# Performance work log

Hardware: AMD Instinct MI355X
Metric: run time of the kernel (lower is better)

The kernel has to match this reference:

```python
import jax, jax.numpy as jnp
import numpy as np

B, NV, H, D = 8, 16, 192, 512
NH = 8
HD = D // NH
DFF = 2048
EPS = 1e-5


def _bn(x, g, b):
    # x: (N, T, C); BatchNorm1d over channel C using batch stats (train mode)
    mu = jnp.mean(x, axis=(0, 1))
    var = jnp.var(x, axis=(0, 1))
    return (x - mu) / jnp.sqrt(var + EPS) * g + b


def _ff(x, w1, b1, w2, b2):
    h = jax.nn.gelu(jnp.einsum('bnhd,fd->bnhf', x, w1) + b1, approximate=False)
    return jnp.einsum('bnhf,df->bnhd', h, w2) + b2


def setup_inputs() -> dict:
    key = jax.random.key(0)
    ks = jax.random.split(key, 20)
    s = 0.02
    return {
        'src': jax.random.normal(ks[0], (B, NV, H, D), jnp.float32),
        'qk_w': jax.random.normal(ks[1], (2 * D, D), jnp.float32) * s,
        'qk_b': jnp.zeros((2 * D,), jnp.float32),
        'v_w': jax.random.normal(ks[2], (D, D), jnp.float32) * s,
        'v_b': jnp.zeros((D,), jnp.float32),
        'alpha_p': jax.random.normal(ks[3], (HD, 1), jnp.float32) * 0.1,
        'g_pre1': jnp.ones((D,), jnp.float32),
        'b_pre1': jnp.zeros((D,), jnp.float32),
        'g_pre2': jnp.ones((D,), jnp.float32),
        'b_pre2': jnp.zeros((D,), jnp.float32),
        'ff1_w1': jax.random.normal(ks[4], (DFF, D), jnp.float32) * s,
        'ff1_b1': jnp.zeros((DFF,), jnp.float32),
        'ff1_w2': jax.random.normal(ks[5], (D, DFF), jnp.float32) * s,
        'ff1_b2': jnp.zeros((D,), jnp.float32),
        'ff2_w1': jax.random.normal(ks[6], (DFF, D), jnp.float32) * s,
        'ff2_b1': jnp.zeros((DFF,), jnp.float32),
        'ff2_w2': jax.random.normal(ks[7], (D, DFF), jnp.float32) * s,
        'ff2_b2': jnp.zeros((D,), jnp.float32),
        'g_attn': jnp.ones((D,), jnp.float32),
        'b_attn': jnp.zeros((D,), jnp.float32),
    }


def reference(src, qk_w, qk_b, v_w, v_b, alpha_p,
              g_pre1, b_pre1, g_pre2, b_pre2,
              ff1_w1, ff1_b1, ff1_w2, ff1_b2,
              ff2_w1, ff2_b1, ff2_w2, ff2_b2,
              g_attn, b_attn):
    b, n, h, c = src.shape
    hd = c // NH
    # normalized input for q,k; raw for v
    src1 = src / jnp.linalg.norm(src, axis=-1, keepdims=True)
    qk = (jnp.einsum('bnhc,ec->bnhe', src1, qk_w) + qk_b)
    qk = qk.reshape(b, n, h, 2, NH, hd).transpose(3, 0, 1, 4, 2, 5)  # (2,b,n,NH,h,hd)
    q, k = qk[0], qk[1]
    v = (jnp.einsum('bnhc,ec->bnhe', src, v_w) + v_b)
    v = v.reshape(b, n, h, NH, hd).transpose(0, 1, 3, 2, 4)  # (b,n,NH,h,hd)

    # exponential-decay weights in FFT domain (branch: h != 7)
    a = jax.nn.sigmoid(alpha_p)                  # (hd,1)
    ar = jnp.arange(h - 1, -1, -1, dtype=src.dtype)
    weights = a * (1.0 - a) ** ar                # (hd, h)
    n2 = 2 * h
    w_f = jnp.fft.rfft(weights, n=n2, axis=-1)   # (hd, h+1)
    q_f = jnp.swapaxes(jnp.fft.rfft(q, n=n2, axis=-2), -1, -2) * w_f
    k_f = jnp.swapaxes(jnp.fft.rfft(k, n=n2, axis=-2), -1, -2) * w_f
    q1 = jnp.swapaxes(jnp.fft.irfft(q_f, n=n2, axis=-1)[..., :h], -1, -2)
    k1 = jnp.swapaxes(jnp.fft.irfft(k_f, n=n2, axis=-1)[..., :h], -1, -2)

    # token-axis attention (note: original divides by head_dim**-0.5 == * sqrt(hd))
    score_t = jnp.einsum('bnhed,bnhfd->bnhef', q1, k1) * (hd ** 0.5)
    attn_t = jax.nn.softmax(score_t, axis=-1)
    out_tok = jnp.einsum('bnhef,bnhfd->bnhed', attn_t, v)  # (b,n,NH,h,hd)
    o3 = _bn(out_tok.reshape(b * n, h, NH * hd), g_pre2, b_pre2).reshape(b, n, h, c)

    # hidden-axis attention on un-decayed q,k (scale = sqrt(h))
    score_h = jnp.einsum('bnhae,bnhaf->bnhef', q, k) * (h ** 0.5)
    attn_h = jax.nn.softmax(score_h, axis=-1)
    out_hid = jnp.einsum('bnhef,bnhaf->bnhae', attn_h, v)  # (b,n,NH,h,hd)
    o2 = _bn(out_hid.reshape(b * n, h, NH * hd), g_pre1, b_pre1).reshape(b, n, h, c)

    src2 = _ff(o3, ff1_w1, ff1_b1, ff1_w2, ff1_b2) + _ff(o2, ff2_w1, ff2_b1, ff2_w2, ff2_b2)
    out = src + src2
    out = _bn(out.reshape(b * n, h, c), g_attn, b_attn).reshape(b, n, h, c)
    return out
```

## Files before the change

kernel.cpp:

```cpp
#include <hip/hip_runtime.h>
#include <math.h>

#define SEQ 192
#define NTOK 24576
#define EPS 1e-5f

typedef __bf16 bf16x8 __attribute__((ext_vector_type(8)));
typedef __bf16 bf16x4 __attribute__((ext_vector_type(4)));
typedef float  f32x4  __attribute__((ext_vector_type(4)));

__device__ __forceinline__ void load_lds16(const __bf16* g, __bf16* l) {
    __builtin_amdgcn_global_load_lds(
        (const __attribute__((address_space(1))) uint32_t*)g,
        (__attribute__((address_space(3))) uint32_t*)l, 16, 0, 0);
}

__device__ __forceinline__ float gelu_f(float x) {
    float z = 1.5957691216057308f * x * fmaf(0.044715f, x*x, 1.f);
    float e = __expf(-z);
    return x * __builtin_amdgcn_rcpf(1.f + e);
}

__global__ __launch_bounds__(256) void cvt_k(const float* __restrict__ x, __bf16* __restrict__ y)
{
    int i = blockIdx.x * 256 + threadIdx.x;
    f32x4 v = ((const f32x4*)x)[i];
    bf16x4 o;
    o[0]=(__bf16)v[0]; o[1]=(__bf16)v[1]; o[2]=(__bf16)v[2]; o[3]=(__bf16)v[3];
    ((bf16x4*)y)[i] = o;
}

__global__ __launch_bounds__(256) void prep_k(const float* __restrict__ src,
    __bf16* __restrict__ srcb, __bf16* __restrict__ srcnb)
{
    int w = threadIdx.x >> 6, lane = threadIdx.x & 63;
    size_t token = blockIdx.x * 4 + w;
    const float* p = src + token * 512 + lane * 8;
    f32x4 a0 = *(const f32x4*)p;
    f32x4 a1 = *(const f32x4*)(p + 4);
    float s = a0[0]*a0[0]+a0[1]*a0[1]+a0[2]*a0[2]+a0[3]*a0[3]
            + a1[0]*a1[0]+a1[1]*a1[1]+a1[2]*a1[2]+a1[3]*a1[3];
#pragma unroll
    for (int off = 32; off; off >>= 1) s += __shfl_xor(s, off);
    float rs = rsqrtf(s);
    bf16x8 vb, vn;
#pragma unroll
    for (int q = 0; q < 4; q++) {
        vb[q]   = (__bf16)a0[q];      vn[q]   = (__bf16)(a0[q]*rs);
        vb[q+4] = (__bf16)a1[q];      vn[q+4] = (__bf16)(a1[q]*rs);
    }
    *(bf16x8*)&srcb[token*512 + lane*8]  = vb;
    *(bf16x8*)&srcnb[token*512 + lane*8] = vn;
}

template<bool AFFINE, bool GELU>
__global__ __launch_bounds__(256) void gemm_k(
    const __bf16* __restrict__ A, const __bf16* __restrict__ B, __bf16* __restrict__ C,
    int N, int K, const float* __restrict__ bias, const float* __restrict__ coef)
{
    __shared__ __bf16 As[8192];
    __shared__ __bf16 Bs[8192];
    const int tid = threadIdx.x, lane = tid & 63, w = tid >> 6;
    const int wr = w >> 1, wc = w & 1;
    const int m0 = blockIdx.y * 128, n0 = blockIdx.x * 128;
    const int fr = lane & 15, fq = lane >> 4;
    const int grow = 8*w + (lane >> 3);
    const int gcol = ((lane & 7) ^ (lane >> 3)) * 8;
    const __bf16* gB = B + (size_t)(n0 + grow) * K + gcol;
    const __bf16* gA = A + (size_t)(m0 + grow) * K + gcol;
    __bf16* ldsA = As + 8*w*64 + lane*8;
    __bf16* ldsB = Bs + 8*w*64 + lane*8;

    f32x4 acc[4][4];
#pragma unroll
    for (int i = 0; i < 4; i++)
#pragma unroll
        for (int j = 0; j < 4; j++) acc[i][j] = (f32x4){0.f,0.f,0.f,0.f};

    for (int k0 = 0; k0 < K; k0 += 64) {
        if (!AFFINE) {
#pragma unroll
            for (int i = 0; i < 4; i++)
                load_lds16(gA + k0 + (size_t)(32*i)*K, ldsA + i*2048);
        } else {
            const int r = tid >> 3, cseg = tid & 7;
            const float* scp = coef + k0 + cseg*8;
            const float* shp = coef + 512 + k0 + cseg*8;
            f32x4 sc0 = *(const f32x4*)scp, sc1 = *(const f32x4*)(scp+4);
            f32x4 sh0 = *(const f32x4*)shp, sh1 = *(const f32x4*)(shp+4);
#pragma unroll
            for (int i = 0; i < 4; i++) {
                int row = 32*i + r;
                bf16x8 a = *(const bf16x8*)&A[(size_t)(m0+row)*512 + k0 + cseg*8];
                bf16x8 v;
#pragma unroll
                for (int q = 0; q < 4; q++) {
                    v[q]   = (__bf16)fmaf((float)a[q],   sc0[q], sh0[q]);
                    v[q+4] = (__bf16)fmaf((float)a[q+4], sc1[q], sh1[q]);
                }
                *(bf16x8*)&As[row*64 + ((cseg ^ (r & 7)) * 8)] = v;
            }
        }
#pragma unroll
        for (int i = 0; i < 4; i++)
            load_lds16(gB + k0 + (size_t)(32*i)*K, ldsB + i*2048);
        __syncthreads();
#pragma unroll
        for (int kk = 0; kk < 2; kk++) {
            bf16x8 af[4], bfv[4];
#pragma unroll
            for (int i = 0; i < 4; i++)
                af[i] = *(bf16x8*)&As[(wr*64 + i*16 + fr)*64 + (((kk*4+fq) ^ (fr&7))*8)];
#pragma unroll
            for (int j = 0; j < 4; j++)
                bfv[j] = *(bf16x8*)&Bs[(wc*64 + j*16 + fr)*64 + (((kk*4+fq) ^ (fr&7))*8)];
#pragma unroll
            for (int i = 0; i < 4; i++)
#pragma unroll
                for (int j = 0; j < 4; j++)
                    acc[i][j] = __builtin_amdgcn_mfma_f32_16x16x32_bf16(af[i], bfv[j], acc[i][j], 0, 0, 0);
        }
        __syncthreads();
    }
    const int r4 = lane >> 4, cc = lane & 15;
#pragma unroll
    for (int i = 0; i < 4; i++) {
#pragma unroll
        for (int r = 0; r < 4; r++) {
            int m = m0 + wr*64 + i*16 + r4*4 + r;
#pragma unroll
            for (int j = 0; j < 4; j++) {
                int n = n0 + wc*64 + j*16 + cc;
                float v = acc[i][j][r] + bias[n];
                if (GELU) v = gelu_f(v);
                C[(size_t)m * N + n] = (__bf16)v;
            }
        }
    }
}

__global__ __launch_bounds__(256) void gemm2_k(
    const __bf16* __restrict__ A1, const __bf16* __restrict__ A2,
    const __bf16* __restrict__ B1, const __bf16* __restrict__ B2,
    float* __restrict__ C, const float* __restrict__ b1, const float* __restrict__ b2,
    const float* __restrict__ resid, float* __restrict__ st)
{
    __shared__ __bf16 As[8192];
    __shared__ __bf16 Bs[8192];
    const int tid = threadIdx.x, lane = tid & 63, w = tid >> 6;
    const int wr = w >> 1, wc = w & 1;
    const int m0 = blockIdx.y * 128, n0 = blockIdx.x * 128;
    const int fr = lane & 15, fq = lane >> 4;
    const int grow = 8*w + (lane >> 3);
    const int gcol = ((lane & 7) ^ (lane >> 3)) * 8;
    const int K = 2048;
    __bf16* ldsA = As + 8*w*64 + lane*8;
    __bf16* ldsB = Bs + 8*w*64 + lane*8;

    f32x4 acc[4][4];
#pragma unroll
    for (int i = 0; i < 4; i++)
#pragma unroll
        for (int j = 0; j < 4; j++) acc[i][j] = (f32x4){0.f,0.f,0.f,0.f};

#pragma unroll 1
    for (int half = 0; half < 2; half++) {
        const __bf16* gA = (half ? A2 : A1) + (size_t)(m0 + grow) * K + gcol;
        const __bf16* gB = (half ? B2 : B1) + (size_t)(n0 + grow) * K + gcol;
        for (int k0 = 0; k0 < K; k0 += 64) {
#pragma unroll
            for (int i = 0; i < 4; i++) {
                load_lds16(gA + k0 + (size_t)(32*i)*K, ldsA + i*2048);
                load_lds16(gB + k0 + (size_t)(32*i)*K, ldsB + i*2048);
            }
            __syncthreads();
#pragma unroll
            for (int kk = 0; kk < 2; kk++) {
                bf16x8 af[4], bfv[4];
#pragma unroll
                for (int i = 0; i < 4; i++)
                    af[i] = *(bf16x8*)&As[(wr*64 + i*16 + fr)*64 + (((kk*4+fq) ^ (fr&7))*8)];
#pragma unroll
                for (int j = 0; j < 4; j++)
                    bfv[j] = *(bf16x8*)&Bs[(wc*64 + j*16 + fr)*64 + (((kk*4+fq) ^ (fr&7))*8)];
#pragma unroll
                for (int i = 0; i < 4; i++)
#pragma unroll
                    for (int j = 0; j < 4; j++)
                        acc[i][j] = __builtin_amdgcn_mfma_f32_16x16x32_bf16(af[i], bfv[j], acc[i][j], 0, 0, 0);
            }
            __syncthreads();
        }
    }
    const int r4 = lane >> 4, cc = lane & 15;
    float cs[4] = {0,0,0,0}, cq[4] = {0,0,0,0};
#pragma unroll
    for (int i = 0; i < 4; i++) {
#pragma unroll
        for (int r = 0; r < 4; r++) {
            int m = m0 + wr*64 + i*16 + r4*4 + r;
#pragma unroll
            for (int j = 0; j < 4; j++) {
                int n = n0 + wc*64 + j*16 + cc;
                size_t idx = (size_t)m * 512 + n;
                float v = acc[i][j][r] + b1[n] + b2[n] + resid[idx];
                C[idx] = v;
                cs[j] += v; cq[j] = fmaf(v, v, cq[j]);
            }
        }
    }
#pragma unroll
    for (int j = 0; j < 4; j++) {
        cs[j] += __shfl_xor(cs[j], 16); cs[j] += __shfl_xor(cs[j], 32);
        cq[j] += __shfl_xor(cq[j], 16); cq[j] += __shfl_xor(cq[j], 32);
    }
    if (r4 == 0) {
#pragma unroll
        for (int j = 0; j < 4; j++) {
            int n = n0 + wc*64 + j*16 + cc;
            atomicAdd(&st[n], cs[j]);
            atomicAdd(&st[512 + n], cq[j]);
        }
    }
}

__global__ __launch_bounds__(256) void decay_scan_k(__bf16* __restrict__ QKb, const float* __restrict__ alpha)
{
    int g = blockIdx.x * 256 + threadIdx.x;
    int bn = g >> 10, e = g & 1023;
    float a = 1.f / (1.f + expf(-alpha[e & 63]));
    float rr = 1.f - a;
    __bf16* p = QKb + (size_t)bn * SEQ * 1024 + e;
    float P = 0.f, pw = 1.f;
    for (int t = 0; t < SEQ; t++) {
        P += pw * (float)p[(size_t)t*1024];
        p[(size_t)t*1024] = (__bf16)P;
        pw *= rr;
    }
    float f = a;
    for (int t = SEQ-1; t >= 0; t--) {
        p[(size_t)t*1024] = (__bf16)((float)p[(size_t)t*1024] * f);
        f *= rr;
    }
}

__global__ __launch_bounds__(256) void hidden_attn_mfma_k(
    const __bf16* __restrict__ QKb, const __bf16* __restrict__ Vb, __bf16* __restrict__ OHb)
{
    __shared__ __bf16 smem[25600];
    __bf16* Qt = smem;
    __bf16* Kt = smem + 12800;
    __bf16* Ps = smem;
    __bf16* Vs = smem + 4608;
    const int bn = blockIdx.x >> 3, nh = blockIdx.x & 7;
    const int tid = threadIdx.x, lane = tid & 63, w = tid >> 6;
    const int fr = lane & 15, fq = lane >> 4;
    const size_t rowbase = (size_t)bn * SEQ;

    for (int i = tid; i < 12288; i += 256) {
        int t = i >> 6, j = i & 63;
        const __bf16* g = QKb + (rowbase + t)*1024 + nh*64 + j;
        Qt[j*200 + t] = g[0];
        Kt[j*200 + t] = g[512];
    }
    __syncthreads();

    f32x4 acc[4];
#pragma unroll
    for (int i = 0; i < 4; i++) acc[i] = (f32x4){0.f,0.f,0.f,0.f};
#pragma unroll
    for (int kc = 0; kc < 6; kc++) {
        bf16x8 a = *(bf16x8*)&Qt[(w*16 + fr)*200 + kc*32 + fq*8];
#pragma unroll
        for (int nt = 0; nt < 4; nt++) {
            bf16x8 b = *(bf16x8*)&Kt[(nt*16 + fr)*200 + kc*32 + fq*8];
            acc[nt] = __builtin_amdgcn_mfma_f32_16x16x32_bf16(a, b, acc[nt], 0, 0, 0);
        }
    }
    const float sc = 13.856406460551018f;
    float pn[4][4];
#pragma unroll
    for (int reg = 0; reg < 4; reg++) {
        float m = -1e30f;
#pragma unroll
        for (int nt = 0; nt < 4; nt++) { acc[nt][reg] *= sc; m = fmaxf(m, acc[nt][reg]); }
#pragma unroll
        for (int off = 1; off < 16; off <<= 1) m = fmaxf(m, __shfl_xor(m, off));
        float l = 0.f;
#pragma unroll
        for (int nt = 0; nt < 4; nt++) { pn[nt][reg] = __expf(acc[nt][reg] - m); l += pn[nt][reg]; }
#pragma unroll
        for (int off = 1; off < 16; off <<= 1) l += __shfl_xor(l, off);
        float inv = 1.f / l;
#pragma unroll
        for (int nt = 0; nt < 4; nt++) pn[nt][reg] *= inv;
    }
    __syncthreads();
#pragma unroll
    for (int nt = 0; nt < 4; nt++)
#pragma unroll
        for (int reg = 0; reg < 4; reg++)
            Ps[(w*16 + fq*4 + reg)*72 + nt*16 + fr] = (__bf16)pn[nt][reg];
    for (int i = tid; i < 1536; i += 256) {
        int t = i >> 3, s = i & 7;
        *(bf16x8*)&Vs[t*72 + s*8] = *(const bf16x8*)&Vb[(rowbase+t)*512 + nh*64 + s*8];
    }
    __syncthreads();

    f32x4 o[3][4];
#pragma unroll
    for (int i = 0; i < 3; i++)
#pragma unroll
        for (int j = 0; j < 4; j++) o[i][j] = (f32x4){0.f,0.f,0.f,0.f};
#pragma unroll
    for (int kc = 0; kc < 2; kc++) {
        bf16x8 av[3];
#pragma unroll
        for (int mt = 0; mt < 3; mt++)
            av[mt] = *(bf16x8*)&Vs[(48*w + mt*16 + fr)*72 + kc*32 + fq*8];
#pragma unroll
        for (int nt = 0; nt < 4; nt++) {
            bf16x8 b = *(bf16x8*)&Ps[(nt*16 + fr)*72 + kc*32 + fq*8];
#pragma unroll
            for (int mt = 0; mt < 3; mt++)
                o[mt][nt] = __builtin_amdgcn_mfma_f32_16x16x32_bf16(av[mt], b, o[mt][nt], 0, 0, 0);
        }
    }
    __bf16* obase = OHb + ((size_t)(bn*8 + nh)) * SEQ * 64;
#pragma unroll
    for (int mt = 0; mt < 3; mt++)
#pragma unroll
        for (int reg = 0; reg < 4; reg++) {
            int t = 48*w + mt*16 + fq*4 + reg;
#pragma unroll
            for (int nt = 0; nt < 4; nt++)
                obase[(size_t)t*64 + nt*16 + fr] = (__bf16)o[mt][nt][reg];
        }
}

__global__ __launch_bounds__(256) void token_attn_mfma_k(
    const __bf16* __restrict__ QKb, const __bf16* __restrict__ Vb, __bf16* __restrict__ OT)
{
    __shared__ __bf16 smem[27648];
    __bf16* Qs = smem;
    __bf16* Ks = smem + 13824;
    __bf16* Vt = smem;
    __bf16* Pw = smem + 12800;
    const int bn = blockIdx.x >> 3, nh = blockIdx.x & 7;
    const int tid = threadIdx.x, lane = tid & 63, w = tid >> 6;
    const int fr = lane & 15, fq = lane >> 4;
    const size_t rowbase = (size_t)bn * SEQ;

    for (int i = tid; i < 1536; i += 256) {
        int t = i >> 3, s = i & 7;
        const __bf16* g = QKb + (rowbase + t)*1024 + nh*64;
        *(bf16x8*)&Qs[t*72 + s*8] = *(const bf16x8*)&g[s*8];
        *(bf16x8*)&Ks[t*72 + s*8] = *(const bf16x8*)&g[512 + s*8];
    }
    __syncthreads();

    f32x4 S[3][12];
#pragma unroll
    for (int i = 0; i < 3; i++)
#pragma unroll
        for (int j = 0; j < 12; j++) S[i][j] = (f32x4){0.f,0.f,0.f,0.f};
#pragma unroll
    for (int kc = 0; kc < 2; kc++) {
        bf16x8 aq[3];
#pragma unroll
        for (int mt = 0; mt < 3; mt++)
            aq[mt] = *(bf16x8*)&Qs[(48*w + mt*16 + fr)*72 + kc*32 + fq*8];
#pragma unroll
        for (int nt = 0; nt < 12; nt++) {
            bf16x8 b = *(bf16x8*)&Ks[(nt*16 + fr)*72 + kc*32 + fq*8];
#pragma unroll
            for (int mt = 0; mt < 3; mt++)
                S[mt][nt] = __builtin_amdgcn_mfma_f32_16x16x32_bf16(aq[mt], b, S[mt][nt], 0, 0, 0);
        }
    }
#pragma unroll
    for (int mt = 0; mt < 3; mt++)
#pragma unroll
        for (int reg = 0; reg < 4; reg++) {
            float m = -1e30f;
#pragma unroll
            for (int nt = 0; nt < 12; nt++) { S[mt][nt][reg] *= 8.f; m = fmaxf(m, S[mt][nt][reg]); }
#pragma unroll
            for (int off = 1; off < 16; off <<= 1) m = fmaxf(m, __shfl_xor(m, off));
            float l = 0.f;
#pragma unroll
            for (int nt = 0; nt < 12; nt++) { S[mt][nt][reg] = __expf(S[mt][nt][reg] - m); l += S[mt][nt][reg]; }
#pragma unroll
            for (int off = 1; off < 16; off <<= 1) l += __shfl_xor(l, off);
            float inv = 1.f / l;
#pragma unroll
            for (int nt = 0; nt < 12; nt++) S[mt][nt][reg] *= inv;
        }
    __syncthreads();
    for (int i = tid; i < 12288; i += 256) {
        int t = i >> 6, d = i & 63;
        Vt[d*200 + t] = Vb[(rowbase + t)*512 + nh*64 + d];
    }
    __syncthreads();

    f32x4 O[3][4];
#pragma unroll
    for (int i = 0; i < 3; i++)
#pragma unroll
        for (int j = 0; j < 4; j++) O[i][j] = (f32x4){0.f,0.f,0.f,0.f};
    __bf16* myP = Pw + w*3456;
#pragma unroll
    for (int fc = 0; fc < 3; fc++) {
#pragma unroll
        for (int mt = 0; mt < 3; mt++)
#pragma unroll
            for (int j = 0; j < 4; j++)
#pragma unroll
                for (int reg = 0; reg < 4; reg++)
                    myP[(mt*16 + fq*4 + reg)*72 + j*16 + fr] = (__bf16)S[mt][fc*4 + j][reg];
#pragma unroll
        for (int kc = 0; kc < 2; kc++) {
            bf16x8 ap[3];
#pragma unroll
            for (int mt = 0; mt < 3; mt++)
                ap[mt] = *(bf16x8*)&myP[(mt*16 + fr)*72 + kc*32 + fq*8];
#pragma unroll
            for (int dt = 0; dt < 4; dt++) {
                bf16x8 b = *(bf16x8*)&Vt[(dt*16 + fr)*200 + fc*64 + kc*32 + fq*8];
#pragma unroll
                for (int mt = 0; mt < 3; mt++)
                    O[mt][dt] = __builtin_amdgcn_mfma_f32_16x16x32_bf16(ap[mt], b, O[mt][dt], 0, 0, 0);
            }
        }
    }
    __bf16* obase = OT + ((size_t)(bn*8 + nh)) * SEQ * 64;
#pragma unroll
    for (int mt = 0; mt < 3; mt++)
#pragma unroll
        for (int reg = 0; reg < 4; reg++) {
            int e = 48*w + mt*16 + fq*4 + reg;
#pragma unroll
            for (int dt = 0; dt < 4; dt++)
                obase[(size_t)e*64 + dt*16 + fr] = (__bf16)O[mt][dt][reg];
        }
}

__global__ __launch_bounds__(256) void bn_stats1_k(const __bf16* __restrict__ x, float* __restrict__ part)
{
    __shared__ float red[3072];
    const int col8 = threadIdx.x & 63;
    const int rl   = threadIdx.x >> 6;
    const size_t r0 = (size_t)blockIdx.x * 96;
    f32x4 sA = {0,0,0,0}, sB = {0,0,0,0}, qA = {0,0,0,0}, qB = {0,0,0,0};
    for (int r = rl; r < 96; r += 4) {
        bf16x8 v = *(const bf16x8*)&x[(r0 + r)*512 + col8*8];
        f32x4 lo = { (float)v[0], (float)v[1], (float)v[2], (float)v[3] };
        f32x4 hi = { (float)v[4], (float)v[5], (float)v[6], (float)v[7] };
        sA += lo; sB += hi;
        qA += lo*lo; qB += hi*hi;
    }
    if (rl > 0) {
        float* p = &red[(rl-1)*1024];
        *(f32x4*)&p[col8*8]       = sA;  *(f32x4*)&p[col8*8 + 4]       = sB;
        *(f32x4*)&p[512 + col8*8] = qA;  *(f32x4*)&p[512 + col8*8 + 4] = qB;
    }
    __syncthreads();
    if (rl == 0) {
#pragma unroll
        for (int k = 0; k < 3; k++) {
            float* p = &red[k*1024];
            sA += *(f32x4*)&p[col8*8];       sB += *(f32x4*)&p[col8*8 + 4];
            qA += *(f32x4*)&p[512 + col8*8]; qB += *(f32x4*)&p[512 + col8*8 + 4];
        }
        float* o = &part[(size_t)blockIdx.x * 1024];
        *(f32x4*)&o[col8*8]       = sA;  *(f32x4*)&o[col8*8 + 4]       = sB;
        *(f32x4*)&o[512 + col8*8] = qA;  *(f32x4*)&o[512 + col8*8 + 4] = qB;
    }
}

__global__ __launch_bounds__(256) void bn_stats2_k(const float* __restrict__ part, float* __restrict__ st)
{
    int c = blockIdx.x * 256 + threadIdx.x;
    float s0 = 0.f, s1 = 0.f, s2 = 0.f, s3 = 0.f;
    for (int b = 0; b < 256; b += 4) {
        s0 += part[(size_t)b*1024 + c];
        s1 += part[(size_t)(b+1)*1024 + c];
        s2 += part[(size_t)(b+2)*1024 + c];
        s3 += part[(size_t)(b+3)*1024 + c];
    }
    st[c] = (s0 + s1) + (s2 + s3);
}

__global__ void bn_coef_k(const float* __restrict__ st, const float* __restrict__ g,
                          const float* __restrict__ b, float* __restrict__ coef)
{
    int c = threadIdx.x;
    float mean = st[c] * (1.f/24576.f);
    float var  = st[512+c] * (1.f/24576.f) - mean*mean;
    float sc = rsqrtf(var + EPS) * g[c];
    coef[c] = sc;
    coef[512 + c] = b[c] - mean * sc;
}

__global__ __launch_bounds__(256) void bn_apply4_k(const float* __restrict__ x, const float* __restrict__ st,
    const float* __restrict__ g, const float* __restrict__ b, float* __restrict__ out)
{
    size_t i = (size_t)blockIdx.x * 256 + threadIdx.x;
    int col4 = i & 127;
    f32x4 v = ((const f32x4*)x)[i];
    f32x4 sm = ((const f32x4*)st)[col4];
    f32x4 sq = ((const f32x4*)(st + 512))[col4];
    f32x4 o;
#pragma unroll
    for (int j = 0; j < 4; j++) {
        int c = col4*4 + j;
        float mean = sm[j] * (1.f/24576.f);
        float var  = sq[j] * (1.f/24576.f) - mean*mean;
        o[j] = (v[j] - mean) * rsqrtf(var + EPS) * g[c] + b[c];
    }
    ((f32x4*)out)[i] = o;
}

extern "C" void kernel_launch(void* const* d_in, const int* in_sizes, int n_in,
                              void* d_out, int out_size, void* d_ws, size_t ws_size,
                              hipStream_t stream)
{
    const float* src    = (const float*)d_in[0];
    const float* qk_w   = (const float*)d_in[1];
    const float* qk_b   = (const float*)d_in[2];
    const float* v_w    = (const float*)d_in[3];
    const float* v_b    = (const float*)d_in[4];
    const float* alpha  = (const float*)d_in[5];
    const float* g_pre1 = (const float*)d_in[6];
    const float* b_pre1 = (const float*)d_in[7];
    const float* g_pre2 = (const float*)d_in[8];
    const float* b_pre2 = (const float*)d_in[9];
    const float* ff1_w1 = (const float*)d_in[10];
    const float* ff1_b1 = (const float*)d_in[11];
    const float* ff1_w2 = (const float*)d_in[12];
    const float* ff1_b2 = (const float*)d_in[13];
    const float* ff2_w1 = (const float*)d_in[14];
    const float* ff2_b1 = (const float*)d_in[15];
    const float* ff2_w2 = (const float*)d_in[16];
    const float* ff2_b2 = (const float*)d_in[17];
    const float* g_attn = (const float*)d_in[18];
    const float* b_attn = (const float*)d_in[19];
    float* out = (float*)d_out;

    __bf16* wq   = (__bf16*)d_ws;
    __bf16* wv   = wq  + 524288;
    __bf16* w11  = wv  + 262144;
    __bf16* w12  = w11 + 1048576;
    __bf16* w21  = w12 + 1048576;
    __bf16* w22  = w21 + 1048576;
    __bf16* srcb  = w22 + 1048576;
    __bf16* srcnb = srcb + (size_t)NTOK*512;
    __bf16* QKb   = srcnb + (size_t)NTOK*512;
    __bf16* Vb    = QKb + (size_t)NTOK*1024;
    __bf16* OHbf  = Vb + (size_t)NTOK*512;
    __bf16* o3bf  = OHbf + (size_t)NTOK*512;
    float*  stats = (float*)(o3bf + (size_t)NTOK*512);
    float*  coef0 = stats + 3072;
    float*  coef1 = coef0 + 1024;
    float*  part0 = coef1 + 1024;
    float*  part1 = part0 + 262144;
    __bf16* H1 = srcb;
    __bf16* H2 = H1 + (size_t)12288*2048;
    float *st0 = stats, *st1 = stats + 1024, *st2 = stats + 2048;

    hipMemsetAsync(st2, 0, 1024*sizeof(float), stream);

    cvt_k<<<512,  256, 0, stream>>>(qk_w,   wq);
    cvt_k<<<256,  256, 0, stream>>>(v_w,    wv);
    cvt_k<<<1024, 256, 0, stream>>>(ff1_w1, w11);
    cvt_k<<<1024, 256, 0, stream>>>(ff1_w2, w12);
    cvt_k<<<1024, 256, 0, stream>>>(ff2_w1, w21);
    cvt_k<<<1024, 256, 0, stream>>>(ff2_w2, w22);
    prep_k<<<NTOK/4, 256, 0, stream>>>(src, srcb, srcnb);

    gemm_k<false,false><<<dim3(8, 192), 256, 0, stream>>>(srcnb, wq, QKb, 1024, 512, qk_b, nullptr);
    gemm_k<false,false><<<dim3(4, 192), 256, 0, stream>>>(srcb,  wv, Vb,  512,  512, v_b,  nullptr);

    hidden_attn_mfma_k<<<1024, 256, 0, stream>>>(QKb, Vb, OHbf);

    decay_scan_k<<<512, 256, 0, stream>>>(QKb, alpha);
    token_attn_mfma_k<<<1024, 256, 0, stream>>>(QKb, Vb, o3bf);

    bn_stats1_k<<<256, 256, 0, stream>>>(o3bf, part0);
    bn_stats1_k<<<256, 256, 0, stream>>>(OHbf, part1);
    bn_stats2_k<<<4, 256, 0, stream>>>(part0, st0);
    bn_stats2_k<<<4, 256, 0, stream>>>(part1, st1);
    bn_coef_k<<<1, 512, 0, stream>>>(st0, g_pre2, b_pre2, coef0);
    bn_coef_k<<<1, 512, 0, stream>>>(st1, g_pre1, b_pre1, coef1);

    for (int ch = 0; ch < 2; ch++) {
        size_t off = (size_t)ch * 12288 * 512;
        gemm_k<true,true><<<dim3(16, 96), 256, 0, stream>>>(o3bf + off, w11, H1, 2048, 512, ff1_b1, coef0);
        gemm_k<true,true><<<dim3(16, 96), 256, 0, stream>>>(OHbf + off, w21, H2, 2048, 512, ff2_b1, coef1);
        gemm2_k<<<dim3(4, 96), 256, 0, stream>>>(H1, H2, w12, w22, out + off,
                                                 ff1_b2, ff2_b2, src + off, st2);
    }

    bn_apply4_k<<<12288, 256, 0, stream>>>(out, st2, g_attn, b_attn, out);
}
```

Baseline: 786.8 us.

## Remap GEMM blocks per XCD, shrink gemm2 tile, vectorize scans and transposes

Several independent changes are bundled. The six weight-conversion launches are merged into one kernel. The GEMM block indices are remapped so that consecutive M-rows land on the same XCD, which should improve L2 reuse. gemm2 now uses 64-row tiles and a 1D grid of 768 blocks to raise occupancy and block count. The decay scan handles four channels per thread with vector loads, and the Q/K/V transposes into LDS now pack 8 tokens into one 16-byte LDS store. The risks are fewer blocks in the decay scan and strided global reads in the transposes.

```diff
diff --git a/kernel.cpp b/kernel.cpp
--- a/kernel.cpp
+++ b/kernel.cpp
@@ -21,13 +21,24 @@
     return x * __builtin_amdgcn_rcpf(1.f + e);
 }
 
-__global__ __launch_bounds__(256) void cvt_k(const float* __restrict__ x, __bf16* __restrict__ y)
+__global__ __launch_bounds__(256) void cvtall_k(
+    const float* __restrict__ s0, const float* __restrict__ s1, const float* __restrict__ s2,
+    const float* __restrict__ s3, const float* __restrict__ s4, const float* __restrict__ s5,
+    __bf16* __restrict__ dst)
 {
     int i = blockIdx.x * 256 + threadIdx.x;
-    f32x4 v = ((const f32x4*)x)[i];
+    int f = i * 4;
+    const float* s; int off;
+    if      (f <  524288) { s = s0; off = 0;       }
+    else if (f <  786432) { s = s1; off = 524288;  }
+    else if (f < 1835008) { s = s2; off = 786432;  }
+    else if (f < 2883584) { s = s3; off = 1835008; }
+    else if (f < 3932160) { s = s4; off = 2883584; }
+    else                  { s = s5; off = 3932160; }
+    f32x4 v = *(const f32x4*)&s[f - off];
     bf16x4 o;
     o[0]=(__bf16)v[0]; o[1]=(__bf16)v[1]; o[2]=(__bf16)v[2]; o[3]=(__bf16)v[3];
-    ((bf16x4*)y)[i] = o;
+    ((bf16x4*)dst)[i] = o;
 }
 
 __global__ __launch_bounds__(256) void prep_k(const float* __restrict__ src,
@@ -62,7 +73,11 @@
     __shared__ __bf16 Bs[8192];
     const int tid = threadIdx.x, lane = tid & 63, w = tid >> 6;
     const int wr = w >> 1, wc = w & 1;
-    const int m0 = blockIdx.y * 128, n0 = blockIdx.x * 128;
+    const int b = blockIdx.y * gridDim.x + blockIdx.x;
+    const int xcd = b & 7, bi = b >> 3;
+    const int ypx = gridDim.y >> 3;
+    const int m0 = (xcd * ypx + bi / gridDim.x) * 128;
+    const int n0 = (bi % gridDim.x) * 128;
     const int fr = lane & 15, fq = lane >> 4;
     const int grow = 8*w + (lane >> 3);
     const int gcol = ((lane & 7) ^ (lane >> 3)) * 8;
@@ -145,11 +160,14 @@
     float* __restrict__ C, const float* __restrict__ b1, const float* __restrict__ b2,
     const float* __restrict__ resid, float* __restrict__ st)
 {
-    __shared__ __bf16 As[8192];
+    __shared__ __bf16 As[4096];
     __shared__ __bf16 Bs[8192];
     const int tid = threadIdx.x, lane = tid & 63, w = tid >> 6;
     const int wr = w >> 1, wc = w & 1;
-    const int m0 = blockIdx.y * 128, n0 = blockIdx.x * 128;
+    const int vb = blockIdx.x;
+    const int xcd = vb & 7, k2 = vb >> 3;
+    const int m0 = (xcd*24 + (k2 >> 2)) * 64;
+    const int n0 = (k2 & 3) * 128;
     const int fr = lane & 15, fq = lane >> 4;
     const int grow = 8*w + (lane >> 3);
     const int gcol = ((lane & 7) ^ (lane >> 3)) * 8;
@@ -157,9 +175,9 @@
     __bf16* ldsA = As + 8*w*64 + lane*8;
     __bf16* ldsB = Bs + 8*w*64 + lane*8;
 
-    f32x4 acc[4][4];
-#pragma unroll
-    for (int i = 0; i < 4; i++)
+    f32x4 acc[2][4];
+#pragma unroll
+    for (int i = 0; i < 2; i++)
 #pragma unroll
         for (int j = 0; j < 4; j++) acc[i][j] = (f32x4){0.f,0.f,0.f,0.f};
 
@@ -168,23 +186,23 @@
         const __bf16* gA = (half ? A2 : A1) + (size_t)(m0 + grow) * K + gcol;
         const __bf16* gB = (half ? B2 : B1) + (size_t)(n0 + grow) * K + gcol;
         for (int k0 = 0; k0 < K; k0 += 64) {
-#pragma unroll
-            for (int i = 0; i < 4; i++) {
-                load_lds16(gA + k0 + (size_t)(32*i)*K, ldsA + i*2048);
+            load_lds16(gA + k0,                 ldsA);
+            load_lds16(gA + k0 + (size_t)32*K,  ldsA + 2048);
+#pragma unroll
+            for (int i = 0; i < 4; i++)
                 load_lds16(gB + k0 + (size_t)(32*i)*K, ldsB + i*2048);
-            }
             __syncthreads();
 #pragma unroll
             for (int kk = 0; kk < 2; kk++) {
-                bf16x8 af[4], bfv[4];
-#pragma unroll
-                for (int i = 0; i < 4; i++)
-                    af[i] = *(bf16x8*)&As[(wr*64 + i*16 + fr)*64 + (((kk*4+fq) ^ (fr&7))*8)];
+                bf16x8 af[2], bfv[4];
+#pragma unroll
+                for (int i = 0; i < 2; i++)
+                    af[i] = *(bf16x8*)&As[(wr*32 + i*16 + fr)*64 + (((kk*4+fq) ^ (fr&7))*8)];
 #pragma unroll
                 for (int j = 0; j < 4; j++)
                     bfv[j] = *(bf16x8*)&Bs[(wc*64 + j*16 + fr)*64 + (((kk*4+fq) ^ (fr&7))*8)];
 #pragma unroll
-                for (int i = 0; i < 4; i++)
+                for (int i = 0; i < 2; i++)
 #pragma unroll
                     for (int j = 0; j < 4; j++)
                         acc[i][j] = __builtin_amdgcn_mfma_f32_16x16x32_bf16(af[i], bfv[j], acc[i][j], 0, 0, 0);
@@ -195,10 +213,10 @@
     const int r4 = lane >> 4, cc = lane & 15;
     float cs[4] = {0,0,0,0}, cq[4] = {0,0,0,0};
 #pragma unroll
-    for (int i = 0; i < 4; i++) {
+    for (int i = 0; i < 2; i++) {
 #pragma unroll
         for (int r = 0; r < 4; r++) {
-            int m = m0 + wr*64 + i*16 + r4*4 + r;
+            int m = m0 + wr*32 + i*16 + r4*4 + r;
 #pragma unroll
             for (int j = 0; j < 4; j++) {
                 int n = n0 + wc*64 + j*16 + cc;
@@ -227,19 +245,30 @@
 __global__ __launch_bounds__(256) void decay_scan_k(__bf16* __restrict__ QKb, const float* __restrict__ alpha)
 {
     int g = blockIdx.x * 256 + threadIdx.x;
-    int bn = g >> 10, e = g & 1023;
-    float a = 1.f / (1.f + expf(-alpha[e & 63]));
-    float rr = 1.f - a;
-    __bf16* p = QKb + (size_t)bn * SEQ * 1024 + e;
-    float P = 0.f, pw = 1.f;
+    int bn = g >> 8, e4 = (g & 255) * 4;
+    int ai = e4 & 63;
+    f32x4 a, rr;
+#pragma unroll
+    for (int j = 0; j < 4; j++) { float av = 1.f/(1.f + __expf(-alpha[ai + j])); a[j] = av; rr[j] = 1.f - av; }
+    __bf16* p = QKb + (size_t)bn * SEQ * 1024 + e4;
+    f32x4 P = {0,0,0,0}, pw = {1,1,1,1};
     for (int t = 0; t < SEQ; t++) {
-        P += pw * (float)p[(size_t)t*1024];
-        p[(size_t)t*1024] = (__bf16)P;
+        bf16x4 v = *(bf16x4*)&p[(size_t)t*1024];
+        f32x4 vf = { (float)v[0], (float)v[1], (float)v[2], (float)v[3] };
+        P += pw * vf;
+        bf16x4 o;
+#pragma unroll
+        for (int j = 0; j < 4; j++) o[j] = (__bf16)P[j];
+        *(bf16x4*)&p[(size_t)t*1024] = o;
         pw *= rr;
     }
-    float f = a;
+    f32x4 f = a;
     for (int t = SEQ-1; t >= 0; t--) {
-        p[(size_t)t*1024] = (__bf16)((float)p[(size_t)t*1024] * f);
+        bf16x4 v = *(bf16x4*)&p[(size_t)t*1024];
+        bf16x4 o;
+#pragma unroll
+        for (int j = 0; j < 4; j++) o[j] = (__bf16)((float)v[j] * f[j]);
+        *(bf16x4*)&p[(size_t)t*1024] = o;
         f *= rr;
     }
 }
@@ -257,11 +286,16 @@
     const int fr = lane & 15, fq = lane >> 4;
     const size_t rowbase = (size_t)bn * SEQ;
 
-    for (int i = tid; i < 12288; i += 256) {
-        int t = i >> 6, j = i & 63;
-        const __bf16* g = QKb + (rowbase + t)*1024 + nh*64 + j;
-        Qt[j*200 + t] = g[0];
-        Kt[j*200 + t] = g[512];
+#pragma unroll
+    for (int it = 0; it < 12; it++) {
+        int tk = tid + (it % 6) * 256;
+        int j = tk & 63, tg = tk >> 6;
+        const __bf16* gsrc = QKb + (rowbase + tg*8)*1024 + nh*64 + j + (it >= 6 ? 512 : 0);
+        bf16x8 v;
+#pragma unroll
+        for (int u = 0; u < 8; u++) v[u] = gsrc[(size_t)u*1024];
+        __bf16* dst = (it >= 6 ? Kt : Qt) + j*200 + tg*8;
+        *(bf16x8*)dst = v;
     }
     __syncthreads();
 
@@ -397,9 +431,15 @@
             for (int nt = 0; nt < 12; nt++) S[mt][nt][reg] *= inv;
         }
     __syncthreads();
-    for (int i = tid; i < 12288; i += 256) {
-        int t = i >> 6, d = i & 63;
-        Vt[d*200 + t] = Vb[(rowbase + t)*512 + nh*64 + d];
+#pragma unroll
+    for (int it = 0; it < 6; it++) {
+        int tk = tid + it * 256;
+        int d = tk & 63, tg = tk >> 6;
+        const __bf16* gsrc = Vb + (rowbase + tg*8)*512 + nh*64 + d;
+        bf16x8 v;
+#pragma unroll
+        for (int u = 0; u < 8; u++) v[u] = gsrc[(size_t)u*512];
+        *(bf16x8*)&Vt[d*200 + tg*8] = v;
     }
     __syncthreads();
 
@@ -570,12 +610,7 @@
 
     hipMemsetAsync(st2, 0, 1024*sizeof(float), stream);
 
-    cvt_k<<<512,  256, 0, stream>>>(qk_w,   wq);
-    cvt_k<<<256,  256, 0, stream>>>(v_w,    wv);
-    cvt_k<<<1024, 256, 0, stream>>>(ff1_w1, w11);
-    cvt_k<<<1024, 256, 0, stream>>>(ff1_w2, w12);
-    cvt_k<<<1024, 256, 0, stream>>>(ff2_w1, w21);
-    cvt_k<<<1024, 256, 0, stream>>>(ff2_w2, w22);
+    cvtall_k<<<4864, 256, 0, stream>>>(qk_w, v_w, ff1_w1, ff1_w2, ff2_w1, ff2_w2, wq);
     prep_k<<<NTOK/4, 256, 0, stream>>>(src, srcb, srcnb);
 
     gemm_k<false,false><<<dim3(8, 192), 256, 0, stream>>>(srcnb, wq, QKb, 1024, 512, qk_b, nullptr);
@@ -583,7 +618,7 @@
 
     hidden_attn_mfma_k<<<1024, 256, 0, stream>>>(QKb, Vb, OHbf);
 
-    decay_scan_k<<<512, 256, 0, stream>>>(QKb, alpha);
+    decay_scan_k<<<128, 256, 0, stream>>>(QKb, alpha);
     token_attn_mfma_k<<<1024, 256, 0, stream>>>(QKb, Vb, o3bf);
 
     bn_stats1_k<<<256, 256, 0, stream>>>(o3bf, part0);
@@ -597,8 +632,8 @@
         size_t off = (size_t)ch * 12288 * 512;
         gemm_k<true,true><<<dim3(16, 96), 256, 0, stream>>>(o3bf + off, w11, H1, 2048, 512, ff1_b1, coef0);
         gemm_k<true,true><<<dim3(16, 96), 256, 0, stream>>>(OHbf + off, w21, H2, 2048, 512, ff2_b1, coef1);
-        gemm2_k<<<dim3(4, 96), 256, 0, stream>>>(H1, H2, w12, w22, out + off,
-                                                 ff1_b2, ff2_b2, src + off, st2);
+        gemm2_k<<<768, 256, 0, stream>>>(H1, H2, w12, w22, out + off,
+                                         ff1_b2, ff2_b2, src + off, st2);
     }
 
     bn_apply4_k<<<12288, 256, 0, stream>>>(out, st2, g_attn, b_attn, out);
```

After: 708.6 us. -9.9%, faster.
